# Optimization experiments

Hardware: AMD Instinct MI355X
Metric: run time of the kernel (lower is better)

## Reference

```python
import jax, jax.numpy as jnp
import numpy as np

N_ROWS = 8388608          # multiple of 4, as required by the chunked linear
N_SEGMENTS = 4096


def setup_inputs() -> dict:
    key = jax.random.key(0)
    kx, ks = jax.random.split(key)
    x = jax.random.normal(kx, (N_ROWS, 4), dtype=jnp.float32)
    # monotone segment boundaries: 0 = slices[0] <= ... <= slices[-1] = N_ROWS
    interior = jnp.sort(jax.random.randint(ks, (N_SEGMENTS - 1,), 1, N_ROWS, dtype=jnp.int32))
    slices = jnp.concatenate([jnp.zeros((1,), jnp.int32), interior,
                              jnp.full((1,), N_ROWS, jnp.int32)])
    # fixed weight from the original module: arange(16).reshape(4, 4)
    W = jnp.arange(16, dtype=jnp.float32).reshape(4, 4)
    return {"x": x, "slices": slices, "W": W}


def reference(x, slices, W):
    # Chunked 4-row linear == plain matmul with the same weight (nn.Linear: y = x @ W.T)
    y = x @ W.T                                           # [N, 4]
    n = y.shape[0]
    # segment id of each row: number of boundaries <= row index, minus 1
    seg = jnp.searchsorted(slices, jnp.arange(n, dtype=slices.dtype), side="right") - 1
    seg = jnp.clip(seg, 0, N_SEGMENTS - 1)
    # per-segment sum of |y| over all elements (rows and features)
    seg_abs = jax.ops.segment_sum(jnp.abs(y).sum(-1), seg, num_segments=N_SEGMENTS)  # [S]
    return y / seg_abs[seg][:, None]
```

## Files before the change

### kernel.cpp

```cpp
#include <hip/hip_runtime.h>


#define NSEG  4096
#define BLK   256
#define RPT   16
#define BATCH 8
#define CHUNK (BLK * RPT)

typedef float v4 __attribute__((ext_vector_type(4)));

__device__ __forceinline__ float absrow(v4 v, const float* w) {
    float y0 = fabsf(v.x * w[0]  + v.y * w[1]  + v.z * w[2]  + v.w * w[3]);
    float y1 = fabsf(v.x * w[4]  + v.y * w[5]  + v.z * w[6]  + v.w * w[7]);
    float y2 = fabsf(v.x * w[8]  + v.y * w[9]  + v.z * w[10] + v.w * w[11]);
    float y3 = fabsf(v.x * w[12] + v.y * w[13] + v.z * w[14] + v.w * w[15]);
    return (y0 + y1) + (y2 + y3);
}

__global__ __launch_bounds__(BLK) void seg_pass1(
    const v4* __restrict__ x, const int* __restrict__ slices,
    const float* __restrict__ W, float* __restrict__ seg_abs, int n)
{
    __shared__ int   sl[NSEG + 1];
    __shared__ float hist[NSEG];
#pragma unroll
    for (int i = threadIdx.x; i < NSEG + 1; i += BLK) sl[i] = slices[i];
#pragma unroll
    for (int i = threadIdx.x; i < NSEG; i += BLK) hist[i] = 0.0f;

    float w[16];
#pragma unroll
    for (int i = 0; i < 16; ++i) w[i] = W[i];
    __syncthreads();

    const int base = blockIdx.x * CHUNK + threadIdx.x;

    int lo = 0, hi = NSEG;
    {
        int r0 = (base < n) ? base : (n - 1);
        while (hi - lo > 1) { int mid = (lo + hi) >> 1; if (sl[mid] <= r0) lo = mid; else hi = mid; }
    }
    int seg = lo;
    float acc = 0.0f;

    const bool full = (base + (RPT - 1) * BLK) < n;
    if (full) {
#pragma unroll
        for (int b = 0; b < RPT / BATCH; ++b) {
            v4 d[BATCH];
#pragma unroll
            for (int j = 0; j < BATCH; ++j)
                d[j] = x[base + (b * BATCH + j) * BLK];
#pragma unroll
            for (int j = 0; j < BATCH; ++j) {
                int r = base + (b * BATCH + j) * BLK;
                int s = seg;
                while (s < NSEG - 1 && sl[s + 1] <= r) ++s;
                if (s != seg) { atomicAdd(&hist[seg], acc); acc = 0.0f; seg = s; }
                acc += absrow(d[j], w);
            }
        }
    } else {
        for (int it = 0; it < RPT; ++it) {
            int r = base + it * BLK;
            if (r < n) {
                int s = seg;
                while (s < NSEG - 1 && sl[s + 1] <= r) ++s;
                if (s != seg) { atomicAdd(&hist[seg], acc); acc = 0.0f; seg = s; }
                acc += absrow(x[r], w);
            }
        }
    }
    if (acc != 0.0f) atomicAdd(&hist[seg], acc);
    __syncthreads();

#pragma unroll
    for (int i = threadIdx.x; i < NSEG; i += BLK) {
        float h = hist[i];
        if (h != 0.0f) atomicAdd(&seg_abs[i], h);
    }
}

__global__ __launch_bounds__(BLK) void seg_pass2(
    const v4* __restrict__ x, const int* __restrict__ slices,
    const float* __restrict__ W, const float* __restrict__ seg_abs,
    v4* __restrict__ out, int n)
{
    __shared__ int sl[NSEG + 1];
#pragma unroll
    for (int i = threadIdx.x; i < NSEG + 1; i += BLK) sl[i] = slices[i];

    float w[16];
#pragma unroll
    for (int i = 0; i < 16; ++i) w[i] = W[i];
    __syncthreads();

    const int base = blockIdx.x * CHUNK + threadIdx.x;

    int lo = 0, hi = NSEG;
    {
        int r0 = (base < n) ? base : (n - 1);
        while (hi - lo > 1) { int mid = (lo + hi) >> 1; if (sl[mid] <= r0) lo = mid; else hi = mid; }
    }
    int seg = lo;
    float inv = 1.0f / seg_abs[seg];

    const bool full = (base + (RPT - 1) * BLK) < n;
    if (full) {
#pragma unroll
        for (int b = 0; b < RPT / BATCH; ++b) {
            v4 d[BATCH];
#pragma unroll
            for (int j = 0; j < BATCH; ++j)
                d[j] = x[base + (b * BATCH + j) * BLK];
#pragma unroll
            for (int j = 0; j < BATCH; ++j) {
                int r = base + (b * BATCH + j) * BLK;
                int s = seg;
                while (s < NSEG - 1 && sl[s + 1] <= r) ++s;
                if (s != seg) { seg = s; inv = 1.0f / seg_abs[seg]; }
                v4 v = d[j], o;
                o.x = (v.x * w[0]  + v.y * w[1]  + v.z * w[2]  + v.w * w[3])  * inv;
                o.y = (v.x * w[4]  + v.y * w[5]  + v.z * w[6]  + v.w * w[7])  * inv;
                o.z = (v.x * w[8]  + v.y * w[9]  + v.z * w[10] + v.w * w[11]) * inv;
                o.w = (v.x * w[12] + v.y * w[13] + v.z * w[14] + v.w * w[15]) * inv;
                __builtin_nontemporal_store(o, &out[r]);
            }
        }
    } else {
        for (int it = 0; it < RPT; ++it) {
            int r = base + it * BLK;
            if (r < n) {
                int s = seg;
                while (s < NSEG - 1 && sl[s + 1] <= r) ++s;
                if (s != seg) { seg = s; inv = 1.0f / seg_abs[seg]; }
                v4 v = x[r], o;
                o.x = (v.x * w[0]  + v.y * w[1]  + v.z * w[2]  + v.w * w[3])  * inv;
                o.y = (v.x * w[4]  + v.y * w[5]  + v.z * w[6]  + v.w * w[7])  * inv;
                o.z = (v.x * w[8]  + v.y * w[9]  + v.z * w[10] + v.w * w[11]) * inv;
                o.w = (v.x * w[12] + v.y * w[13] + v.z * w[14] + v.w * w[15]) * inv;
                __builtin_nontemporal_store(o, &out[r]);
            }
        }
    }
}

extern "C" void kernel_launch(void* const* d_in, const int* in_sizes, int n_in,
                              void* d_out, int out_size, void* d_ws, size_t ws_size,
                              hipStream_t stream) {
    const v4*   x      = (const v4*)d_in[0];
    const int*  slices = (const int*)d_in[1];
    const float* W     = (const float*)d_in[2];
    float*      seg_abs = (float*)d_ws;
    v4*         out    = (v4*)d_out;
    int n = in_sizes[0] / 4;

    hipMemsetAsync(d_ws, 0, NSEG * sizeof(float), stream);

    int nblocks = (n + CHUNK - 1) / CHUNK;
    seg_pass1<<<nblocks, BLK, 0, stream>>>(x, slices, W, seg_abs, n);
    seg_pass2<<<nblocks, BLK, 0, stream>>>(x, slices, W, seg_abs, out, n);
}
```

Measured before the change: 266.9 us.

## Fuse both passes into one persistent cooperative kernel with grid sync

Merges the histogram pass and the normalize pass into a single cooperative kernel with 1024 persistent blocks. Each block loops over chunks, accumulates into its shared-memory histogram, flushes it to global memory, then grid-syncs before normalizing. This removes a kernel launch and the repeated slices load per block, and cuts global atomic flushes from one per chunk-block to one per persistent block. In exchange it adds grid-barrier overhead and caps parallelism at 1024 blocks, and x is still read twice from memory.

```diff
diff --git a/kernel.cpp b/kernel.cpp
--- a/kernel.cpp
+++ b/kernel.cpp
@@ -1,4 +1,7 @@
 #include <hip/hip_runtime.h>
+#include <hip/hip_cooperative_groups.h>
+
+namespace cg = cooperative_groups;
 
 
 #define NSEG  4096
@@ -6,6 +9,7 @@
 #define RPT   16
 #define BATCH 8
 #define CHUNK (BLK * RPT)
+#define NB    1024
 
 typedef float v4 __attribute__((ext_vector_type(4)));
 
@@ -17,9 +21,10 @@
     return (y0 + y1) + (y2 + y3);
 }
 
-__global__ __launch_bounds__(BLK) void seg_pass1(
+__global__ __launch_bounds__(BLK, 4) void seg_fused(
     const v4* __restrict__ x, const int* __restrict__ slices,
-    const float* __restrict__ W, float* __restrict__ seg_abs, int n)
+    const float* __restrict__ W, float* __restrict__ seg_abs,
+    v4* __restrict__ out, int n, int nchunks)
 {
     __shared__ int   sl[NSEG + 1];
     __shared__ float hist[NSEG];
@@ -33,45 +38,47 @@
     for (int i = 0; i < 16; ++i) w[i] = W[i];
     __syncthreads();
 
-    const int base = blockIdx.x * CHUNK + threadIdx.x;
+    for (int c = blockIdx.x; c < nchunks; c += NB) {
+        const int base = c * CHUNK + threadIdx.x;
 
-    int lo = 0, hi = NSEG;
-    {
-        int r0 = (base < n) ? base : (n - 1);
-        while (hi - lo > 1) { int mid = (lo + hi) >> 1; if (sl[mid] <= r0) lo = mid; else hi = mid; }
-    }
-    int seg = lo;
-    float acc = 0.0f;
+        int lo = 0, hi = NSEG;
+        {
+            int r0 = (base < n) ? base : (n - 1);
+            while (hi - lo > 1) { int mid = (lo + hi) >> 1; if (sl[mid] <= r0) lo = mid; else hi = mid; }
+        }
+        int seg = lo;
+        float acc = 0.0f;
 
-    const bool full = (base + (RPT - 1) * BLK) < n;
-    if (full) {
+        const bool full = (base + (RPT - 1) * BLK) < n;
+        if (full) {
 #pragma unroll
-        for (int b = 0; b < RPT / BATCH; ++b) {
-            v4 d[BATCH];
+            for (int b = 0; b < RPT / BATCH; ++b) {
+                v4 d[BATCH];
 #pragma unroll
-            for (int j = 0; j < BATCH; ++j)
-                d[j] = x[base + (b * BATCH + j) * BLK];
+                for (int j = 0; j < BATCH; ++j)
+                    d[j] = x[base + (b * BATCH + j) * BLK];
 #pragma unroll
-            for (int j = 0; j < BATCH; ++j) {
-                int r = base + (b * BATCH + j) * BLK;
-                int s = seg;
-                while (s < NSEG - 1 && sl[s + 1] <= r) ++s;
-                if (s != seg) { atomicAdd(&hist[seg], acc); acc = 0.0f; seg = s; }
-                acc += absrow(d[j], w);
+                for (int j = 0; j < BATCH; ++j) {
+                    int r = base + (b * BATCH + j) * BLK;
+                    int s = seg;
+                    while (s < NSEG - 1 && sl[s + 1] <= r) ++s;
+                    if (s != seg) { atomicAdd(&hist[seg], acc); acc = 0.0f; seg = s; }
+                    acc += absrow(d[j], w);
+                }
+            }
+        } else {
+            for (int it = 0; it < RPT; ++it) {
+                int r = base + it * BLK;
+                if (r < n) {
+                    int s = seg;
+                    while (s < NSEG - 1 && sl[s + 1] <= r) ++s;
+                    if (s != seg) { atomicAdd(&hist[seg], acc); acc = 0.0f; seg = s; }
+                    acc += absrow(x[r], w);
+                }
             }
         }
-    } else {
-        for (int it = 0; it < RPT; ++it) {
-            int r = base + it * BLK;
-            if (r < n) {
-                int s = seg;
-                while (s < NSEG - 1 && sl[s + 1] <= r) ++s;
-                if (s != seg) { atomicAdd(&hist[seg], acc); acc = 0.0f; seg = s; }
-                acc += absrow(x[r], w);
-            }
-        }
+        if (acc != 0.0f) atomicAdd(&hist[seg], acc);
     }
-    if (acc != 0.0f) atomicAdd(&hist[seg], acc);
     __syncthreads();
 
 #pragma unroll
@@ -79,67 +86,63 @@
         float h = hist[i];
         if (h != 0.0f) atomicAdd(&seg_abs[i], h);
     }
-}
 
-__global__ __launch_bounds__(BLK) void seg_pass2(
-    const v4* __restrict__ x, const int* __restrict__ slices,
-    const float* __restrict__ W, const float* __restrict__ seg_abs,
-    v4* __restrict__ out, int n)
-{
-    __shared__ int sl[NSEG + 1];
+    __threadfence();
+    cg::this_grid().sync();
+
+    for (int c = blockIdx.x; c < nchunks; c += NB) {
+        const int base = c * CHUNK + threadIdx.x;
+
+        int lo = 0, hi = NSEG;
+        {
+            int r0 = (base < n) ? base : (n - 1);
+            while (hi - lo > 1) { int mid = (lo + hi) >> 1; if (sl[mid] <= r0) lo = mid; else hi = mid; }
+        }
+        int seg = lo;
+        float inv = 1.0f / __hip_atomic_load(&seg_abs[seg], __ATOMIC_RELAXED, __HIP_MEMORY_SCOPE_AGENT);
+
+        const bool full = (base + (RPT - 1) * BLK) < n;
+        if (full) {
 #pragma unroll
-    for (int i = threadIdx.x; i < NSEG + 1; i += BLK) sl[i] = slices[i];
-
-    float w[16];
+            for (int b = 0; b < RPT / BATCH; ++b) {
+                v4 d[BATCH];
 #pragma unroll
-    for (int i = 0; i < 16; ++i) w[i] = W[i];
-    __syncthreads();
-
-    const int base = blockIdx.x * CHUNK + threadIdx.x;
-
-    int lo = 0, hi = NSEG;
-    {
-        int r0 = (base < n) ? base : (n - 1);
-        while (hi - lo > 1) { int mid = (lo + hi) >> 1; if (sl[mid] <= r0) lo = mid; else hi = mid; }
-    }
-    int seg = lo;
-    float inv = 1.0f / seg_abs[seg];
-
-    const bool full = (base + (RPT - 1) * BLK) < n;
-    if (full) {
+                for (int j = 0; j < BATCH; ++j)
+                    d[j] = x[base + (b * BATCH + j) * BLK];
 #pragma unroll
-        for (int b = 0; b < RPT / BATCH; ++b) {
-            v4 d[BATCH];
-#pragma unroll
-            for (int j = 0; j < BATCH; ++j)
-                d[j] = x[base + (b * BATCH + j) * BLK];
-#pragma unroll
-            for (int j = 0; j < BATCH; ++j) {
-                int r = base + (b * BATCH + j) * BLK;
-                int s = seg;
-                while (s < NSEG - 1 && sl[s + 1] <= r) ++s;
-                if (s != seg) { seg = s; inv = 1.0f / seg_abs[seg]; }
-                v4 v = d[j], o;
-                o.x = (v.x * w[0]  + v.y * w[1]  + v.z * w[2]  + v.w * w[3])  * inv;
-                o.y = (v.x * w[4]  + v.y * w[5]  + v.z * w[6]  + v.w * w[7])  * inv;
-                o.z = (v.x * w[8]  + v.y * w[9]  + v.z * w[10] + v.w * w[11]) * inv;
-                o.w = (v.x * w[12] + v.y * w[13] + v.z * w[14] + v.w * w[15]) * inv;
-                __builtin_nontemporal_store(o, &out[r]);
+                for (int j = 0; j < BATCH; ++j) {
+                    int r = base + (b * BATCH + j) * BLK;
+                    int s = seg;
+                    while (s < NSEG - 1 && sl[s + 1] <= r) ++s;
+                    if (s != seg) {
+                        seg = s;
+                        inv = 1.0f / __hip_atomic_load(&seg_abs[seg], __ATOMIC_RELAXED, __HIP_MEMORY_SCOPE_AGENT);
+                    }
+                    v4 v = d[j], o;
+                    o.x = (v.x * w[0]  + v.y * w[1]  + v.z * w[2]  + v.w * w[3])  * inv;
+                    o.y = (v.x * w[4]  + v.y * w[5]  + v.z * w[6]  + v.w * w[7])  * inv;
+                    o.z = (v.x * w[8]  + v.y * w[9]  + v.z * w[10] + v.w * w[11]) * inv;
+                    o.w = (v.x * w[12] + v.y * w[13] + v.z * w[14] + v.w * w[15]) * inv;
+                    __builtin_nontemporal_store(o, &out[r]);
+                }
             }
-        }
-    } else {
-        for (int it = 0; it < RPT; ++it) {
-            int r = base + it * BLK;
-            if (r < n) {
-                int s = seg;
-                while (s < NSEG - 1 && sl[s + 1] <= r) ++s;
-                if (s != seg) { seg = s; inv = 1.0f / seg_abs[seg]; }
-                v4 v = x[r], o;
-                o.x = (v.x * w[0]  + v.y * w[1]  + v.z * w[2]  + v.w * w[3])  * inv;
-                o.y = (v.x * w[4]  + v.y * w[5]  + v.z * w[6]  + v.w * w[7])  * inv;
-                o.z = (v.x * w[8]  + v.y * w[9]  + v.z * w[10] + v.w * w[11]) * inv;
-                o.w = (v.x * w[12] + v.y * w[13] + v.z * w[14] + v.w * w[15]) * inv;
-                __builtin_nontemporal_store(o, &out[r]);
+        } else {
+            for (int it = 0; it < RPT; ++it) {
+                int r = base + it * BLK;
+                if (r < n) {
+                    int s = seg;
+                    while (s < NSEG - 1 && sl[s + 1] <= r) ++s;
+                    if (s != seg) {
+                        seg = s;
+                        inv = 1.0f / __hip_atomic_load(&seg_abs[seg], __ATOMIC_RELAXED, __HIP_MEMORY_SCOPE_AGENT);
+                    }
+                    v4 v = x[r], o;
+                    o.x = (v.x * w[0]  + v.y * w[1]  + v.z * w[2]  + v.w * w[3])  * inv;
+                    o.y = (v.x * w[4]  + v.y * w[5]  + v.z * w[6]  + v.w * w[7])  * inv;
+                    o.z = (v.x * w[8]  + v.y * w[9]  + v.z * w[10] + v.w * w[11]) * inv;
+                    o.w = (v.x * w[12] + v.y * w[13] + v.z * w[14] + v.w * w[15]) * inv;
+                    __builtin_nontemporal_store(o, &out[r]);
+                }
             }
         }
     }
@@ -148,16 +151,17 @@
 extern "C" void kernel_launch(void* const* d_in, const int* in_sizes, int n_in,
                               void* d_out, int out_size, void* d_ws, size_t ws_size,
                               hipStream_t stream) {
-    const v4*   x      = (const v4*)d_in[0];
-    const int*  slices = (const int*)d_in[1];
-    const float* W     = (const float*)d_in[2];
-    float*      seg_abs = (float*)d_ws;
-    v4*         out    = (v4*)d_out;
+    const v4*    x       = (const v4*)d_in[0];
+    const int*   slices  = (const int*)d_in[1];
+    const float* W       = (const float*)d_in[2];
+    float*       seg_abs = (float*)d_ws;
+    v4*          out     = (v4*)d_out;
     int n = in_sizes[0] / 4;
+    int nchunks = (n + CHUNK - 1) / CHUNK;
 
     hipMemsetAsync(d_ws, 0, NSEG * sizeof(float), stream);
 
-    int nblocks = (n + CHUNK - 1) / CHUNK;
-    seg_pass1<<<nblocks, BLK, 0, stream>>>(x, slices, W, seg_abs, n);
-    seg_pass2<<<nblocks, BLK, 0, stream>>>(x, slices, W, seg_abs, out, n);
+    void* args[] = {(void*)&x, (void*)&slices, (void*)&W, (void*)&seg_abs,
+                    (void*)&out, (void*)&n, (void*)&nchunks};
+    hipLaunchCooperativeKernel((void*)seg_fused, dim3(NB), dim3(BLK), args, 0, stream);
 }
```

New measurement: 503.8 us. 88.7% more time.
